# Optimization experiments

Hardware: AMD Instinct MI355X
Metric: run time of the kernel (lower is better)

Reference implementation:

```python
import jax, jax.numpy as jnp
import numpy as np

DIM = 192
WIN = (7, 7)
HEADS = 6
HEAD_DIM = DIM // HEADS
SCALE = HEAD_DIM ** -0.5
N = WIN[0] * WIN[1]  # 49


def _relative_position_index():
    # Faithful to the TF build(): tf.meshgrid uses default 'xy' indexing.
    ch = np.arange(WIN[0])
    cw = np.arange(WIN[1])
    coords = np.stack(np.meshgrid(ch, cw))            # [2, Wh, Ww] (xy indexing)
    flat = coords.reshape(2, -1)                      # [2, N]
    rel = flat[:, :, None] - flat[:, None, :]         # [2, N, N]
    rel = rel.transpose(1, 2, 0)                      # [N, N, 2]
    rel = rel + np.array([WIN[0] - 1, WIN[1] - 1])
    rel = rel * np.array([2 * WIN[1] - 1, 1])
    return jnp.asarray(rel.sum(-1), dtype=jnp.int32)  # [N, N]


REL_INDEX = _relative_position_index()


def setup_inputs() -> dict:
    key = jax.random.key(0)
    ks = jax.random.split(key, 8)
    B_ = 4096
    nW = 64
    x = jax.random.normal(ks[0], (B_, N, DIM), dtype=jnp.float32)
    mask = jnp.zeros((nW, N, N), dtype=jnp.float32)
    s = 0.02
    w_qkv = jax.random.truncated_normal(ks[1], -2.0, 2.0, (DIM, 3 * DIM), jnp.float32) * s
    b_qkv = jnp.zeros((3 * DIM,), dtype=jnp.float32)
    w_proj = jax.random.truncated_normal(ks[2], -2.0, 2.0, (DIM, DIM), jnp.float32) * s
    b_proj = jnp.zeros((DIM,), dtype=jnp.float32)
    table = jax.random.truncated_normal(ks[3], -2.0, 2.0, ((2 * WIN[0] - 1) * (2 * WIN[1] - 1), HEADS), jnp.float32) * s
    return {"x": x, "mask": mask, "w_qkv": w_qkv, "b_qkv": b_qkv,
            "w_proj": w_proj, "b_proj": b_proj, "table": table}


def reference(x, mask, w_qkv, b_qkv, w_proj, b_proj, table):
    B_, n, C = x.shape
    qkv = x @ w_qkv + b_qkv                               # [B_, N, 3C]
    qkv = qkv.reshape(B_, n, 3, HEADS, HEAD_DIM).transpose(2, 0, 3, 1, 4)
    q, k, v = qkv[0], qkv[1], qkv[2]                      # [B_, H, N, hd]
    attn = jnp.einsum('bhnd,bhmd->bhnm', q * SCALE, k)    # [B_, H, N, N]
    bias = table[REL_INDEX.reshape(-1)].reshape(n, n, HEADS).transpose(2, 0, 1)
    attn = attn + bias[None]
    nW = mask.shape[0]
    attn = attn.reshape(B_ // nW, nW, HEADS, n, n) + mask[None, :, None]
    attn = attn.reshape(B_, HEADS, n, n)
    attn = jax.nn.softmax(attn, axis=-1)
    out = jnp.einsum('bhnm,bhmd->bhnd', attn, v)          # [B_, H, N, hd]
    out = out.transpose(0, 2, 1, 3).reshape(B_, n, C)
    return out @ w_proj + b_proj
```

## Files before the change

### kernel.cpp

```cpp
#include <hip/hip_runtime.h>
#include <stdint.h>

#define NTOK 49
#define DIM  192
#define QKV3 576
#define NHEADS 6

typedef __attribute__((ext_vector_type(8))) short short8;
typedef __attribute__((ext_vector_type(4))) float f32x4;

__device__ __forceinline__ uint16_t f2bf(float f) {
    uint32_t u = __float_as_uint(f);
    return (uint16_t)((u + 0x7FFFu + ((u >> 16) & 1u)) >> 16);
}
__device__ __forceinline__ uint32_t cvtpk_bf16(float a, float b) {
    uint32_t r;
    asm("v_cvt_pk_bf16_f32 %0, %1, %2" : "=v"(r) : "v"(a), "v"(b));
    return r;
}

__device__ __forceinline__ int swz(int row, int col) {
    return row * 192 + ((((col >> 3) ^ (row & 7)) << 3)) + (col & 7);
}
__device__ __forceinline__ int vswz(int d, int tok) {
    return d * 64 + ((((tok >> 3) ^ (d & 7)) << 3)) + (tok & 7);
}

#define NQ (QKV3 * DIM)
#define NP (DIM * DIM)
#define NB (NHEADS * 4 * 4 * 64 * 4)
#define WS_BASE ((size_t)(NQ + NP) * 2 + (size_t)NB * 4)

__global__ void prep_base(const float* __restrict__ wqkv,
                          const float* __restrict__ wproj,
                          const float* __restrict__ table,
                          uint16_t* __restrict__ ws) {
    int i = blockIdx.x * 256 + threadIdx.x;
    if (i < NQ) {
        int ct   = i / 3072;
        int rem  = i - ct * 3072;
        int kk   = rem >> 9;
        int lane = (rem >> 3) & 63;
        int jj   = rem & 7;
        int col  = ct * 16 + (lane & 15);
        int k    = kk * 32 + (lane >> 4) * 8 + jj;
        ws[i] = f2bf(wqkv[(size_t)k * QKV3 + col]);
    } else if (i < NQ + NP) {
        int j    = i - NQ;
        int hn   = j >> 9;
        int lane = (j >> 3) & 63;
        int jj   = j & 7;
        int h    = hn / 12, nt = hn - h * 12;
        int col  = nt * 16 + (lane & 15);
        int k    = h * 32 + (lane >> 4) * 8 + jj;
        ws[NQ + j] = f2bf(wproj[(size_t)k * DIM + col]);
    } else if (i < NQ + NP + NB) {
        int e    = i - NQ - NP;
        int ii   = e & 3;
        int lane = (e >> 2) & 63;
        int nt   = (e >> 8) & 3;
        int mt   = (e >> 10) & 3;
        int h    = e >> 12;
        int r = mt * 16 + (lane & 15);
        int c = nt * 16 + ((lane >> 4) << 2) + ii;
        float val = 0.f;
        if (r < NTOK && c < NTOK) {
            int rm = r % 7, rd = r / 7, cm = c % 7, cd = c / 7;
            val = table[(13 * (rm - cm + 6) + (rd - cd + 6)) * NHEADS + h];
        }
        ((float*)(ws + NQ + NP))[e] = val;
    }
}

__global__ void prep_fold(const float* __restrict__ mask,
                          const float* __restrict__ table,
                          float* __restrict__ fold) {
    __shared__ float msk[NTOK * NTOK];
    const int wm  = blockIdx.x / (NB / 256);
    const int sub = blockIdx.x % (NB / 256);
    for (int i = threadIdx.x; i < NTOK * NTOK; i += 256)
        msk[i] = mask[(size_t)wm * (NTOK * NTOK) + i];
    __syncthreads();
    int e    = sub * 256 + threadIdx.x;
    int ii   = e & 3;
    int lane = (e >> 2) & 63;
    int nt   = (e >> 8) & 3;
    int mt   = (e >> 10) & 3;
    int h    = e >> 12;
    int r = mt * 16 + (lane & 15);
    int c = nt * 16 + ((lane >> 4) << 2) + ii;
    int qa = (r < NTOK) ? r : (NTOK - 1);
    int ka = (c < NTOK) ? c : (NTOK - 1);
    float val = msk[qa * NTOK + ka];
    if (r < NTOK && c < NTOK) {
        int rm = r % 7, rd = r / 7, cm = c % 7, cd = c / 7;
        val += table[(13 * (rm - cm + 6) + (rd - cd + 6)) * NHEADS + h];
    }
    fold[(size_t)wm * NB + e] = val;
}

#define U_OFF   0
#define QS_OFF  9408
#define KS_OFF  18816
#define VTA_OFF 28224
#define LDS_ELS 40512
#define PA_STR  72
#define R_STR   52

template <int NCT, int PM>
__device__ __forceinline__ void phaseA_pass(uint16_t* lds,
                                            const uint16_t* __restrict__ wqkvP,
                                            const float* __restrict__ w_qkv,
                                            const float* __restrict__ b_qkv,
                                            const int base, const int lane,
                                            const int q4, const int l16)
{
    const float SCALE = 0.17677669529663687f;
    f32x4 acc[NCT][4];
    #pragma unroll
    for (int j = 0; j < NCT; ++j)
        #pragma unroll
        for (int mt = 0; mt < 4; ++mt) acc[j][mt] = (f32x4){0.f, 0.f, 0.f, 0.f};

    #pragma unroll
    for (int kk = 0; kk < 6; ++kk) {
        short8 bf[NCT];
        #pragma unroll
        for (int j = 0; j < NCT; ++j) {
            const int ct = base + 8 * j;
            if (PM >= 1) {
                bf[j] = *(const short8*)&wqkvP[(((size_t)(ct * 6 + kk)) << 9) + (lane << 3)];
            } else {
                union { uint16_t u[8]; short8 v; } tb;
                const int col = ct * 16 + l16;
                const int k0  = kk * 32 + q4 * 8;
                #pragma unroll
                for (int jj = 0; jj < 8; ++jj)
                    tb.u[jj] = f2bf(w_qkv[(size_t)(k0 + jj) * QKV3 + col]);
                bf[j] = tb.v;
            }
        }
        #pragma unroll
        for (int mt = 0; mt < 4; ++mt) {
            short8 af = *(const short8*)&lds[U_OFF + swz(mt * 16 + l16, kk * 32 + q4 * 8)];
            #pragma unroll
            for (int j = 0; j < NCT; ++j)
                acc[j][mt] = __builtin_amdgcn_mfma_f32_16x16x32_bf16(af, bf[j], acc[j][mt], 0, 0, 0);
        }
    }

    #pragma unroll
    for (int j = 0; j < NCT; ++j) {
        const int ct  = base + 8 * j;
        const int col = ct * 16 + l16;
        const float bias = b_qkv[col];
        if (col < DIM) {
            #pragma unroll
            for (int mt = 0; mt < 4; ++mt)
                #pragma unroll
                for (int i = 0; i < 4; ++i) {
                    int tok = mt * 16 + q4 * 4 + i;
                    if (tok < NTOK)
                        lds[QS_OFF + swz(tok, col)] = f2bf((acc[j][mt][i] + bias) * SCALE);
                }
        } else if (col < 2 * DIM) {
            const int kc = col - DIM;
            #pragma unroll
            for (int mt = 0; mt < 4; ++mt)
                #pragma unroll
                for (int i = 0; i < 4; ++i) {
                    int tok = mt * 16 + q4 * 4 + i;
                    if (tok < NTOK)
                        lds[KS_OFF + swz(tok, kc)] = f2bf(acc[j][mt][i] + bias);
                }
        } else {
            const int vc = col - 2 * DIM;
            #pragma unroll
            for (int mt = 0; mt < 4; ++mt) {
                const int tokb = mt * 16 + q4 * 4;
                union { uint16_t u[4]; ushort4 v; } pv;
                #pragma unroll
                for (int i = 0; i < 4; ++i) {
                    int tok = tokb + i;
                    pv.u[i] = (tok < NTOK) ? f2bf(acc[j][mt][i] + bias) : (uint16_t)0;
                }
                *(ushort4*)&lds[VTA_OFF + vc * 64 + ((((tokb >> 3) ^ (vc & 7)) << 3)) + (tokb & 7)] = pv.v;
            }
        }
    }
}

template <int PM>
__global__ __launch_bounds__(512, 4)
void winattn_mfma5(const float* __restrict__ x,
                   const float* __restrict__ mask, int nW,
                   const float* __restrict__ w_qkv,
                   const float* __restrict__ b_qkv,
                   const float* __restrict__ w_proj,
                   const float* __restrict__ b_proj,
                   const float* __restrict__ table,
                   const uint16_t* __restrict__ wpre,
                   const float* __restrict__ fold,
                   float* __restrict__ out)
{
    __shared__ __align__(16) uint16_t lds[LDS_ELS];

    const int b    = blockIdx.x;
    const int t    = threadIdx.x;
    const int wave = t >> 6;
    const int lane = t & 63;
    const int q4   = lane >> 4;
    const int l16  = lane & 15;

    const uint16_t* wqkvP  = wpre;
    const uint16_t* wprojP = wpre + NQ;
    const float*    biasT  = (const float*)(wpre + NQ + NP);
    const float*    maskw  = mask + (size_t)(b % nW) * (NTOK * NTOK);
    const float*    foldw  = (PM == 2) ? (fold + (size_t)(b % nW) * NB) : nullptr;

    {
        const float4* xb = (const float4*)(x + (size_t)b * (NTOK * DIM));
        for (int i = t; i < NTOK * DIM / 4; i += 512) {
            float4 v = xb[i];
            int e = i * 4, row = e / DIM, col = e - row * DIM;
            union { uint16_t u[4]; ushort4 v4; } s;
            s.u[0] = f2bf(v.x); s.u[1] = f2bf(v.y);
            s.u[2] = f2bf(v.z); s.u[3] = f2bf(v.w);
            *(ushort4*)&lds[U_OFF + swz(row, col)] = s.v4;
        }
    }
    __syncthreads();

    phaseA_pass<4, PM>(lds, wqkvP, w_qkv, b_qkv, wave, lane, q4, l16);
    if (wave < 4)
        phaseA_pass<1, PM>(lds, wqkvP, w_qkv, b_qkv, 32 + wave, lane, q4, l16);
    __syncthreads();

    const int mt    = wave & 3;
    const int hbase = (wave >> 2) * 3;
    uint16_t* paw = &lds[U_OFF + wave * (16 * PA_STR)];
    const int qt = mt * 16 + l16;
    const int qa = (qt < NTOK) ? qt : (NTOK - 1);

    f32x4 pacc[12];
    #pragma unroll
    for (int nt = 0; nt < 12; ++nt) pacc[nt] = (f32x4){0.f, 0.f, 0.f, 0.f};

    for (int hi = 0; hi < 3; ++hi) {
        const int h = hbase + hi;
        short8 bq = *(const short8*)&lds[QS_OFF + swz(qt, h * 32 + q4 * 8)];
        f32x4 lg[4];
        __builtin_amdgcn_s_setprio(1);
        #pragma unroll
        for (int nt = 0; nt < 4; ++nt) {
            short8 ak = *(const short8*)&lds[KS_OFF + swz(nt * 16 + l16, h * 32 + q4 * 8)];
            f32x4 z = (f32x4){0.f, 0.f, 0.f, 0.f};
            lg[nt] = __builtin_amdgcn_mfma_f32_16x16x32_bf16(ak, bq, z, 0, 0, 0);
        }
        __builtin_amdgcn_s_setprio(0);
        #pragma unroll
        for (int nt = 0; nt < 4; ++nt) {
            if (PM == 2) {
                f32x4 bb = *(const f32x4*)&foldw[(((h * 4 + mt) * 4 + nt) * 64 + lane) * 4];
                #pragma unroll
                for (int i = 0; i < 4; ++i) lg[nt][i] += bb[i];
            } else if (PM == 1) {
                f32x4 bb = *(const f32x4*)&biasT[(((h * 4 + mt) * 4 + nt) * 64 + lane) * 4];
                #pragma unroll
                for (int i = 0; i < 4; ++i) {
                    int kt = nt * 16 + q4 * 4 + i;
                    int ka = (kt < NTOK) ? kt : (NTOK - 1);
                    lg[nt][i] += bb[i] + maskw[qa * NTOK + ka];
                }
            } else {
                #pragma unroll
                for (int i = 0; i < 4; ++i) {
                    int kt = nt * 16 + q4 * 4 + i;
                    int ka = (kt < NTOK) ? kt : (NTOK - 1);
                    int rm = qa % 7, rd = qa / 7, cm = ka % 7, cd = ka / 7;
                    int bi = 13 * (rm - cm + 6) + (rd - cd + 6);
                    lg[nt][i] += table[bi * NHEADS + h] + maskw[qa * NTOK + ka];
                }
            }
        }
        float m = lg[0][0];
        #pragma unroll
        for (int nt = 0; nt < 3; ++nt)
            #pragma unroll
            for (int i = 0; i < 4; ++i) m = fmaxf(m, lg[nt][i]);
        if (q4 == 0) m = fmaxf(m, lg[3][0]);
        m = fmaxf(m, __shfl_xor(m, 16));
        m = fmaxf(m, __shfl_xor(m, 32));
        float s = 0.f;
        #pragma unroll
        for (int nt = 0; nt < 3; ++nt)
            #pragma unroll
            for (int i = 0; i < 4; ++i) { lg[nt][i] = __expf(lg[nt][i] - m); s += lg[nt][i]; }
        float e30 = (q4 == 0) ? __expf(lg[3][0] - m) : 0.f;
        s += e30;
        s += __shfl_xor(s, 16);
        s += __shfl_xor(s, 32);
        const float inv = 1.f / s;
        #pragma unroll
        for (int nt = 0; nt < 3; ++nt) {
            uint32_t lo = cvtpk_bf16(lg[nt][0] * inv, lg[nt][1] * inv);
            uint32_t hi = cvtpk_bf16(lg[nt][2] * inv, lg[nt][3] * inv);
            uint32_t* dst = (uint32_t*)&paw[l16 * PA_STR + nt * 16 + q4 * 4];
            dst[0] = lo; dst[1] = hi;
        }
        {
            uint32_t lo = cvtpk_bf16(e30 * inv, 0.f);
            uint32_t* dst = (uint32_t*)&paw[l16 * PA_STR + 48 + q4 * 4];
            dst[0] = lo; dst[1] = 0u;
        }
        asm volatile("" ::: "memory");

        f32x4 ov[2];
        ov[0] = (f32x4){0.f, 0.f, 0.f, 0.f};
        ov[1] = (f32x4){0.f, 0.f, 0.f, 0.f};
        __builtin_amdgcn_s_setprio(1);
        #pragma unroll
        for (int kk = 0; kk < 2; ++kk) {
            short8 ap = *(const short8*)&paw[l16 * PA_STR + kk * 32 + q4 * 8];
            #pragma unroll
            for (int n2 = 0; n2 < 2; ++n2) {
                short8 bv = *(const short8*)&lds[VTA_OFF + vswz(h * 32 + n2 * 16 + l16,
                                                                kk * 32 + q4 * 8)];
                ov[n2] = __builtin_amdgcn_mfma_f32_16x16x32_bf16(ap, bv, ov[n2], 0, 0, 0);
            }
        }
        __builtin_amdgcn_s_setprio(0);
        asm volatile("" ::: "memory");
        #pragma unroll
        for (int n2 = 0; n2 < 2; ++n2)
            #pragma unroll
            for (int i = 0; i < 4; ++i)
                paw[(q4 * 4 + i) * PA_STR + n2 * 16 + l16] = f2bf(ov[n2][i]);
        asm volatile("" ::: "memory");

        short8 ap2 = *(const short8*)&paw[l16 * PA_STR + q4 * 8];
        __builtin_amdgcn_s_setprio(1);
        #pragma unroll
        for (int nt = 0; nt < 12; ++nt) {
            short8 bw;
            if (PM >= 1) {
                bw = *(const short8*)&wprojP[(((size_t)(h * 12 + nt)) << 9) + (lane << 3)];
            } else {
                union { uint16_t u[8]; short8 v; } tb;
                int k0 = h * 32 + q4 * 8;
                #pragma unroll
                for (int j = 0; j < 8; ++j)
                    tb.u[j] = f2bf(w_proj[(size_t)(k0 + j) * DIM + nt * 16 + l16]);
                bw = tb.v;
            }
            pacc[nt] = __builtin_amdgcn_mfma_f32_16x16x32_bf16(ap2, bw, pacc[nt], 0, 0, 0);
        }
        __builtin_amdgcn_s_setprio(0);
    }
    __syncthreads();

    float* R = (float*)lds;
    if (wave >= 4) {
        float* rw = R + (size_t)(mt * 64 + lane) * R_STR;
        #pragma unroll
        for (int nt = 0; nt < 12; ++nt)
            *(f32x4*)(rw + nt * 4) = pacc[nt];
    }
    __syncthreads();
    if (wave < 4) {
        const float* rr = R + (size_t)(mt * 64 + lane) * R_STR;
        float* ob = out + (size_t)b * (NTOK * DIM);
        #pragma unroll
        for (int nt = 0; nt < 12; ++nt) {
            f32x4 other = *(const f32x4*)(rr + nt * 4);
            const int c = nt * 16 + l16;
            const float bp = b_proj[c];
            #pragma unroll
            for (int i = 0; i < 4; ++i) {
                const int r = mt * 16 + q4 * 4 + i;
                if (r < NTOK) ob[r * DIM + c] = pacc[nt][i] + other[i] + bp;
            }
        }
    }
}

extern "C" void kernel_launch(void* const* d_in, const int* in_sizes, int n_in,
                              void* d_out, int out_size, void* d_ws, size_t ws_size,
                              hipStream_t stream) {
    const float* x      = (const float*)d_in[0];
    const float* mask   = (const float*)d_in[1];
    const float* w_qkv  = (const float*)d_in[2];
    const float* b_qkv  = (const float*)d_in[3];
    const float* w_proj = (const float*)d_in[4];
    const float* b_proj = (const float*)d_in[5];
    const float* table  = (const float*)d_in[6];
    float* out = (float*)d_out;

    const int nblocks = in_sizes[0] / (NTOK * DIM);
    const int nW      = in_sizes[1] / (NTOK * NTOK);
    const size_t WS_FOLD = (size_t)nW * NB * 4;

    if (d_ws != nullptr && ws_size >= WS_BASE + WS_FOLD) {
        uint16_t* wpre = (uint16_t*)d_ws;
        float* fold = (float*)((char*)d_ws + WS_BASE);
        const int total = NQ + NP + NB;
        prep_base<<<(total + 255) / 256, 256, 0, stream>>>(w_qkv, w_proj, table, wpre);
        prep_fold<<<nW * (NB / 256), 256, 0, stream>>>(mask, table, fold);
        winattn_mfma5<2><<<nblocks, 512, 0, stream>>>(x, mask, nW, w_qkv, b_qkv,
                                                      w_proj, b_proj, table, wpre, fold, out);
    } else if (d_ws != nullptr && ws_size >= WS_BASE) {
        uint16_t* wpre = (uint16_t*)d_ws;
        const int total = NQ + NP + NB;
        prep_base<<<(total + 255) / 256, 256, 0, stream>>>(w_qkv, w_proj, table, wpre);
        winattn_mfma5<1><<<nblocks, 512, 0, stream>>>(x, mask, nW, w_qkv, b_qkv,
                                                      w_proj, b_proj, table, wpre, nullptr, out);
    } else {
        winattn_mfma5<0><<<nblocks, 512, 0, stream>>>(x, mask, nW, w_qkv, b_qkv,
                                                      w_proj, b_proj, table, nullptr, nullptr, out);
    }
}
```

Before: 441.5 us.

## Merge prep kernels, transpose Q/K MFMA epilogue, use packed bf16 stores

Folds the two preprocessing kernels into a single prep_all launch. That kernel also writes a pre-scaled qkv bias and a fragment-ordered mask instead of a per-window folded bias+mask. The Q/K projection MFMAs now swap operands so each lane holds four consecutive columns, which allows packed 8-byte LDS stores via v_cvt_pk_bf16. The x staging and V writes also use packed conversion, and phase A is split per Q/K/V type with sched barriers. The attention logits now need two loads (bias table plus mask) instead of one folded load, which trades a kernel launch and a large fold buffer for extra per-element loads.

New measurement: 413.0 us. 6.5% less time.

```diff
diff --git a/kernel.cpp b/kernel.cpp
--- a/kernel.cpp
+++ b/kernel.cpp
@@ -5,6 +5,7 @@
 #define DIM  192
 #define QKV3 576
 #define NHEADS 6
+#define SCALE_F 0.17677669529663687f
 
 typedef __attribute__((ext_vector_type(8))) short short8;
 typedef __attribute__((ext_vector_type(4))) float f32x4;
@@ -29,12 +30,21 @@
 #define NQ (QKV3 * DIM)
 #define NP (DIM * DIM)
 #define NB (NHEADS * 4 * 4 * 64 * 4)
-#define WS_BASE ((size_t)(NQ + NP) * 2 + (size_t)NB * 4)
-
-__global__ void prep_base(const float* __restrict__ wqkv,
-                          const float* __restrict__ wproj,
-                          const float* __restrict__ table,
-                          uint16_t* __restrict__ ws) {
+#define OFF_BQ ((size_t)(NQ + NP) * 2 + (size_t)NB * 4)
+#define OFF_MF (OFF_BQ + 576 * 4)
+
+__global__ void prep_all(const float* __restrict__ wqkv,
+                         const float* __restrict__ wproj,
+                         const float* __restrict__ table,
+                         const float* __restrict__ bqkv,
+                         const float* __restrict__ mask,
+                         int nmaskels,
+                         uint8_t* __restrict__ wsb) {
+    uint16_t* wq = (uint16_t*)wsb;
+    uint16_t* wp = (uint16_t*)(wsb + (size_t)NQ * 2);
+    float*    bT = (float*)(wsb + (size_t)(NQ + NP) * 2);
+    float*    bq = (float*)(wsb + OFF_BQ);
+    float*    mF = (float*)(wsb + OFF_MF);
     int i = blockIdx.x * 256 + threadIdx.x;
     if (i < NQ) {
         int ct   = i / 3072;
@@ -44,7 +54,7 @@
         int jj   = rem & 7;
         int col  = ct * 16 + (lane & 15);
         int k    = kk * 32 + (lane >> 4) * 8 + jj;
-        ws[i] = f2bf(wqkv[(size_t)k * QKV3 + col]);
+        wq[i] = f2bf(wqkv[(size_t)k * QKV3 + col]);
     } else if (i < NQ + NP) {
         int j    = i - NQ;
         int hn   = j >> 9;
@@ -53,7 +63,7 @@
         int h    = hn / 12, nt = hn - h * 12;
         int col  = nt * 16 + (lane & 15);
         int k    = h * 32 + (lane >> 4) * 8 + jj;
-        ws[NQ + j] = f2bf(wproj[(size_t)k * DIM + col]);
+        wp[j] = f2bf(wproj[(size_t)k * DIM + col]);
     } else if (i < NQ + NP + NB) {
         int e    = i - NQ - NP;
         int ii   = e & 3;
@@ -68,35 +78,23 @@
             int rm = r % 7, rd = r / 7, cm = c % 7, cd = c / 7;
             val = table[(13 * (rm - cm + 6) + (rd - cd + 6)) * NHEADS + h];
         }
-        ((float*)(ws + NQ + NP))[e] = val;
-    }
-}
-
-__global__ void prep_fold(const float* __restrict__ mask,
-                          const float* __restrict__ table,
-                          float* __restrict__ fold) {
-    __shared__ float msk[NTOK * NTOK];
-    const int wm  = blockIdx.x / (NB / 256);
-    const int sub = blockIdx.x % (NB / 256);
-    for (int i = threadIdx.x; i < NTOK * NTOK; i += 256)
-        msk[i] = mask[(size_t)wm * (NTOK * NTOK) + i];
-    __syncthreads();
-    int e    = sub * 256 + threadIdx.x;
-    int ii   = e & 3;
-    int lane = (e >> 2) & 63;
-    int nt   = (e >> 8) & 3;
-    int mt   = (e >> 10) & 3;
-    int h    = e >> 12;
-    int r = mt * 16 + (lane & 15);
-    int c = nt * 16 + ((lane >> 4) << 2) + ii;
-    int qa = (r < NTOK) ? r : (NTOK - 1);
-    int ka = (c < NTOK) ? c : (NTOK - 1);
-    float val = msk[qa * NTOK + ka];
-    if (r < NTOK && c < NTOK) {
-        int rm = r % 7, rd = r / 7, cm = c % 7, cd = c / 7;
-        val += table[(13 * (rm - cm + 6) + (rd - cd + 6)) * NHEADS + h];
-    }
-    fold[(size_t)wm * NB + e] = val;
+        bT[e] = val;
+    } else if (i < NQ + NP + NB + 576) {
+        int e = i - NQ - NP - NB;
+        bq[e] = (e < DIM) ? bqkv[e] * SCALE_F : bqkv[e];
+    } else if (i < NQ + NP + NB + 576 + nmaskels) {
+        int e    = i - NQ - NP - NB - 576;
+        int ii   = e & 3;
+        int lane = (e >> 2) & 63;
+        int nt   = (e >> 8) & 3;
+        int mt   = (e >> 10) & 3;
+        int wm   = e >> 12;
+        int r = mt * 16 + (lane & 15);
+        int c = nt * 16 + ((lane >> 4) << 2) + ii;
+        int qa = (r < NTOK) ? r : (NTOK - 1);
+        int ka = (c < NTOK) ? c : (NTOK - 1);
+        mF[e] = mask[(size_t)wm * (NTOK * NTOK) + qa * NTOK + ka];
+    }
 }
 
 #define U_OFF   0
@@ -107,27 +105,27 @@
 #define PA_STR  72
 #define R_STR   52
 
-template <int NCT, int PM>
-__device__ __forceinline__ void phaseA_pass(uint16_t* lds,
-                                            const uint16_t* __restrict__ wqkvP,
-                                            const float* __restrict__ w_qkv,
-                                            const float* __restrict__ b_qkv,
-                                            const int base, const int lane,
-                                            const int q4, const int l16)
+template <int NCT, int TGT, int PM>
+__device__ __forceinline__ void phaseA_typed(uint16_t* lds,
+                                             const uint16_t* __restrict__ wqkvP,
+                                             const float* __restrict__ w_qkv,
+                                             const float* __restrict__ bqkvF,
+                                             const float* __restrict__ b_qkv,
+                                             const int ct0, const int lane,
+                                             const int q4, const int l16)
 {
-    const float SCALE = 0.17677669529663687f;
     f32x4 acc[NCT][4];
     #pragma unroll
     for (int j = 0; j < NCT; ++j)
         #pragma unroll
-        for (int mt = 0; mt < 4; ++mt) acc[j][mt] = (f32x4){0.f, 0.f, 0.f, 0.f};
+        for (int tt = 0; tt < 4; ++tt) acc[j][tt] = (f32x4){0.f, 0.f, 0.f, 0.f};
 
     #pragma unroll
     for (int kk = 0; kk < 6; ++kk) {
         short8 bf[NCT];
         #pragma unroll
         for (int j = 0; j < NCT; ++j) {
-            const int ct = base + 8 * j;
+            const int ct = ct0 + 8 * j;
             if (PM >= 1) {
                 bf[j] = *(const short8*)&wqkvP[(((size_t)(ct * 6 + kk)) << 9) + (lane << 3)];
             } else {
@@ -141,50 +139,70 @@
             }
         }
         #pragma unroll
-        for (int mt = 0; mt < 4; ++mt) {
-            short8 af = *(const short8*)&lds[U_OFF + swz(mt * 16 + l16, kk * 32 + q4 * 8)];
-            #pragma unroll
-            for (int j = 0; j < NCT; ++j)
-                acc[j][mt] = __builtin_amdgcn_mfma_f32_16x16x32_bf16(af, bf[j], acc[j][mt], 0, 0, 0);
+        for (int tt = 0; tt < 4; ++tt) {
+            short8 af = *(const short8*)&lds[U_OFF + swz(tt * 16 + l16, kk * 32 + q4 * 8)];
+            #pragma unroll
+            for (int j = 0; j < NCT; ++j) {
+                if (TGT <= 1)
+                    acc[j][tt] = __builtin_amdgcn_mfma_f32_16x16x32_bf16(bf[j], af, acc[j][tt], 0, 0, 0);
+                else
+                    acc[j][tt] = __builtin_amdgcn_mfma_f32_16x16x32_bf16(af, bf[j], acc[j][tt], 0, 0, 0);
+            }
         }
     }
 
     #pragma unroll
     for (int j = 0; j < NCT; ++j) {
-        const int ct  = base + 8 * j;
-        const int col = ct * 16 + l16;
-        const float bias = b_qkv[col];
-        if (col < DIM) {
-            #pragma unroll
-            for (int mt = 0; mt < 4; ++mt)
-                #pragma unroll
-                for (int i = 0; i < 4; ++i) {
-                    int tok = mt * 16 + q4 * 4 + i;
-                    if (tok < NTOK)
-                        lds[QS_OFF + swz(tok, col)] = f2bf((acc[j][mt][i] + bias) * SCALE);
+        const int ct = ct0 + 8 * j;
+        if (TGT <= 1) {
+            const int colb = ct * 16 + q4 * 4;
+            f32x4 b4;
+            if (PM >= 1) {
+                b4 = *(const f32x4*)&bqkvF[colb];
+            } else {
+                #pragma unroll
+                for (int i = 0; i < 4; ++i)
+                    b4[i] = (TGT == 0) ? b_qkv[colb + i] * SCALE_F : b_qkv[colb + i];
+            }
+            const int lc   = (TGT == 0) ? colb : (colb - DIM);
+            const int base = (TGT == 0) ? QS_OFF : KS_OFF;
+            #pragma unroll
+            for (int tt = 0; tt < 4; ++tt) {
+                const int tok = tt * 16 + l16;
+                float v0, v1, v2, v3;
+                if (TGT == 0) {
+                    v0 = fmaf(acc[j][tt][0], SCALE_F, b4[0]);
+                    v1 = fmaf(acc[j][tt][1], SCALE_F, b4[1]);
+                    v2 = fmaf(acc[j][tt][2], SCALE_F, b4[2]);
+                    v3 = fmaf(acc[j][tt][3], SCALE_F, b4[3]);
+                } else {
+                    v0 = acc[j][tt][0] + b4[0];
+                    v1 = acc[j][tt][1] + b4[1];
+                    v2 = acc[j][tt][2] + b4[2];
+                    v3 = acc[j][tt][3] + b4[3];
                 }
-        } else if (col < 2 * DIM) {
-            const int kc = col - DIM;
-            #pragma unroll
-            for (int mt = 0; mt < 4; ++mt)
-                #pragma unroll
-                for (int i = 0; i < 4; ++i) {
-                    int tok = mt * 16 + q4 * 4 + i;
-                    if (tok < NTOK)
-                        lds[KS_OFF + swz(tok, kc)] = f2bf(acc[j][mt][i] + bias);
-                }
+                uint2 pw;
+                pw.x = cvtpk_bf16(v0, v1);
+                pw.y = cvtpk_bf16(v2, v3);
+                if (tok < NTOK)
+                    *(uint2*)&lds[base + swz(tok, lc)] = pw;
+            }
         } else {
-            const int vc = col - 2 * DIM;
+            const int col = ct * 16 + l16;
+            const int vc  = col - 2 * DIM;
+            const float bias = (PM >= 1) ? bqkvF[col] : b_qkv[col];
             #pragma unroll
             for (int mt = 0; mt < 4; ++mt) {
                 const int tokb = mt * 16 + q4 * 4;
-                union { uint16_t u[4]; ushort4 v; } pv;
-                #pragma unroll
-                for (int i = 0; i < 4; ++i) {
-                    int tok = tokb + i;
-                    pv.u[i] = (tok < NTOK) ? f2bf(acc[j][mt][i] + bias) : (uint16_t)0;
-                }
-                *(ushort4*)&lds[VTA_OFF + vc * 64 + ((((tokb >> 3) ^ (vc & 7)) << 3)) + (tokb & 7)] = pv.v;
+                float z0 = (tokb + 0 < NTOK) ? acc[j][mt][0] + bias : 0.f;
+                float z1 = (tokb + 1 < NTOK) ? acc[j][mt][1] + bias : 0.f;
+                float z2 = (tokb + 2 < NTOK) ? acc[j][mt][2] + bias : 0.f;
+                float z3 = (tokb + 3 < NTOK) ? acc[j][mt][3] + bias : 0.f;
+                uint2 pw;
+                pw.x = cvtpk_bf16(z0, z1);
+                pw.y = cvtpk_bf16(z2, z3);
+                *(uint2*)&lds[VTA_OFF + vc * 64 +
+                              ((((tokb >> 3) ^ (vc & 7)) << 3)) + (tokb & 7)] = pw;
             }
         }
     }
@@ -192,15 +210,14 @@
 
 template <int PM>
 __global__ __launch_bounds__(512, 4)
-void winattn_mfma5(const float* __restrict__ x,
+void winattn_mfma6(const float* __restrict__ x,
                    const float* __restrict__ mask, int nW,
                    const float* __restrict__ w_qkv,
                    const float* __restrict__ b_qkv,
                    const float* __restrict__ w_proj,
                    const float* __restrict__ b_proj,
                    const float* __restrict__ table,
-                   const uint16_t* __restrict__ wpre,
-                   const float* __restrict__ fold,
+                   const uint8_t* __restrict__ wsb,
                    float* __restrict__ out)
 {
     __shared__ __align__(16) uint16_t lds[LDS_ELS];
@@ -212,28 +229,40 @@
     const int q4   = lane >> 4;
     const int l16  = lane & 15;
 
-    const uint16_t* wqkvP  = wpre;
-    const uint16_t* wprojP = wpre + NQ;
-    const float*    biasT  = (const float*)(wpre + NQ + NP);
+    const uint16_t* wqkvP  = (const uint16_t*)wsb;
+    const uint16_t* wprojP = (const uint16_t*)(wsb + (size_t)NQ * 2);
+    const float*    biasT  = (const float*)(wsb + (size_t)(NQ + NP) * 2);
+    const float*    bqkvF  = (const float*)(wsb + OFF_BQ);
+    const float*    maskF  = (const float*)(wsb + OFF_MF);
     const float*    maskw  = mask + (size_t)(b % nW) * (NTOK * NTOK);
-    const float*    foldw  = (PM == 2) ? (fold + (size_t)(b % nW) * NB) : nullptr;
+    const float*    maskFw = maskF + (size_t)(b % nW) * 4096;
 
     {
         const float4* xb = (const float4*)(x + (size_t)b * (NTOK * DIM));
         for (int i = t; i < NTOK * DIM / 4; i += 512) {
             float4 v = xb[i];
             int e = i * 4, row = e / DIM, col = e - row * DIM;
-            union { uint16_t u[4]; ushort4 v4; } s;
-            s.u[0] = f2bf(v.x); s.u[1] = f2bf(v.y);
-            s.u[2] = f2bf(v.z); s.u[3] = f2bf(v.w);
-            *(ushort4*)&lds[U_OFF + swz(row, col)] = s.v4;
+            uint2 s;
+            s.x = cvtpk_bf16(v.x, v.y);
+            s.y = cvtpk_bf16(v.z, v.w);
+            *(uint2*)&lds[U_OFF + swz(row, col)] = s;
         }
     }
     __syncthreads();
 
-    phaseA_pass<4, PM>(lds, wqkvP, w_qkv, b_qkv, wave, lane, q4, l16);
-    if (wave < 4)
-        phaseA_pass<1, PM>(lds, wqkvP, w_qkv, b_qkv, 32 + wave, lane, q4, l16);
+    if (wave < 4) {
+        phaseA_typed<2, 0, PM>(lds, wqkvP, w_qkv, bqkvF, b_qkv, wave,      lane, q4, l16);
+        __builtin_amdgcn_sched_barrier(0);
+        phaseA_typed<1, 1, PM>(lds, wqkvP, w_qkv, bqkvF, b_qkv, 16 + wave, lane, q4, l16);
+        __builtin_amdgcn_sched_barrier(0);
+        phaseA_typed<2, 2, PM>(lds, wqkvP, w_qkv, bqkvF, b_qkv, 24 + wave, lane, q4, l16);
+    } else {
+        phaseA_typed<1, 0, PM>(lds, wqkvP, w_qkv, bqkvF, b_qkv, wave,      lane, q4, l16);
+        __builtin_amdgcn_sched_barrier(0);
+        phaseA_typed<2, 1, PM>(lds, wqkvP, w_qkv, bqkvF, b_qkv, 8 + wave,  lane, q4, l16);
+        __builtin_amdgcn_sched_barrier(0);
+        phaseA_typed<1, 2, PM>(lds, wqkvP, w_qkv, bqkvF, b_qkv, 24 + wave, lane, q4, l16);
+    }
     __syncthreads();
 
     const int mt    = wave & 3;
@@ -261,9 +290,10 @@
         #pragma unroll
         for (int nt = 0; nt < 4; ++nt) {
             if (PM == 2) {
-                f32x4 bb = *(const f32x4*)&foldw[(((h * 4 + mt) * 4 + nt) * 64 + lane) * 4];
-                #pragma unroll
-                for (int i = 0; i < 4; ++i) lg[nt][i] += bb[i];
+                f32x4 bb = *(const f32x4*)&biasT[(((h * 4 + mt) * 4 + nt) * 64 + lane) * 4];
+                f32x4 mm = *(const f32x4*)&maskFw[((mt * 4 + nt) * 64 + lane) * 4];
+                #pragma unroll
+                for (int i = 0; i < 4; ++i) lg[nt][i] += bb[i] + mm[i];
             } else if (PM == 1) {
                 f32x4 bb = *(const f32x4*)&biasT[(((h * 4 + mt) * 4 + nt) * 64 + lane) * 4];
                 #pragma unroll
@@ -398,24 +428,26 @@
 
     const int nblocks = in_sizes[0] / (NTOK * DIM);
     const int nW      = in_sizes[1] / (NTOK * NTOK);
-    const size_t WS_FOLD = (size_t)nW * NB * 4;
-
-    if (d_ws != nullptr && ws_size >= WS_BASE + WS_FOLD) {
-        uint16_t* wpre = (uint16_t*)d_ws;
-        float* fold = (float*)((char*)d_ws + WS_BASE);
-        const int total = NQ + NP + NB;
-        prep_base<<<(total + 255) / 256, 256, 0, stream>>>(w_qkv, w_proj, table, wpre);
-        prep_fold<<<nW * (NB / 256), 256, 0, stream>>>(mask, table, fold);
-        winattn_mfma5<2><<<nblocks, 512, 0, stream>>>(x, mask, nW, w_qkv, b_qkv,
-                                                      w_proj, b_proj, table, wpre, fold, out);
-    } else if (d_ws != nullptr && ws_size >= WS_BASE) {
-        uint16_t* wpre = (uint16_t*)d_ws;
-        const int total = NQ + NP + NB;
-        prep_base<<<(total + 255) / 256, 256, 0, stream>>>(w_qkv, w_proj, table, wpre);
-        winattn_mfma5<1><<<nblocks, 512, 0, stream>>>(x, mask, nW, w_qkv, b_qkv,
-                                                      w_proj, b_proj, table, wpre, nullptr, out);
+    const size_t NEED1 = OFF_MF;
+    const size_t NEED2 = OFF_MF + (size_t)nW * 4096 * 4;
+
+    if (d_ws != nullptr && ws_size >= NEED2) {
+        uint8_t* wsb = (uint8_t*)d_ws;
+        const int nmask = nW * 4096;
+        const int total = NQ + NP + NB + 576 + nmask;
+        prep_all<<<(total + 255) / 256, 256, 0, stream>>>(w_qkv, w_proj, table,
+                                                          b_qkv, mask, nmask, wsb);
+        winattn_mfma6<2><<<nblocks, 512, 0, stream>>>(x, mask, nW, w_qkv, b_qkv,
+                                                      w_proj, b_proj, table, wsb, out);
+    } else if (d_ws != nullptr && ws_size >= NEED1) {
+        uint8_t* wsb = (uint8_t*)d_ws;
+        const int total = NQ + NP + NB + 576;
+        prep_all<<<(total + 255) / 256, 256, 0, stream>>>(w_qkv, w_proj, table,
+                                                          b_qkv, mask, 0, wsb);
+        winattn_mfma6<1><<<nblocks, 512, 0, stream>>>(x, mask, nW, w_qkv, b_qkv,
+                                                      w_proj, b_proj, table, wsb, out);
     } else {
-        winattn_mfma5<0><<<nblocks, 512, 0, stream>>>(x, mask, nW, w_qkv, b_qkv,
-                                                      w_proj, b_proj, table, nullptr, nullptr, out);
-    }
-}
+        winattn_mfma6<0><<<nblocks, 512, 0, stream>>>(x, mask, nW, w_qkv, b_qkv,
+                                                      w_proj, b_proj, table, nullptr, out);
+    }
+}
```
